# Performance work log

Measured on AMD Instinct MI355X. Metric: run time of the kernel, lower is better.

## Reference

```python
import jax, jax.numpy as jnp
import numpy as np
import math

B, Hs, Ws, C, NH, PP = 4, 32, 32, 1024, 16, 128
N = Hs * Ws
HD = C // NH
MAX_REL = 32
ROPE_THETA = 10000.0


def _gelu(t):
    return jax.nn.gelu(t, approximate=False)  # torch nn.GELU default (erf)


def _rope(x):
    # x: [B, nh, N, hd]; interleaved even/odd rotation as in _apply_rope
    hd = x.shape[-1]
    inv_freq = 1.0 / (ROPE_THETA ** (jnp.arange(0, hd, 2, dtype=jnp.float32) / hd))
    pos = jnp.arange(x.shape[-2], dtype=jnp.float32)
    ang = pos[:, None] * inv_freq[None, :]  # [N, hd/2]
    sin, cos = jnp.sin(ang), jnp.cos(ang)
    x1, x2 = x[..., 0::2], x[..., 1::2]
    return jnp.stack([x1 * cos - x2 * sin, x2 * cos + x1 * sin], axis=-1).reshape(x.shape)


def _rel_bias(table):
    # static index computation (numpy), gather from learned table -> [1, NH, N, N]
    coords = np.arange(Hs)
    cy, cx = np.meshgrid(coords, coords, indexing='ij')
    cf = np.stack([cy.reshape(-1), cx.reshape(-1)])  # [2, N]
    rel = cf[:, :, None] - cf[:, None, :]            # [2, N, N]
    idx = (rel[0] + MAX_REL - 1) * (2 * MAX_REL - 1) + (rel[1] + MAX_REL - 1)
    return table[jnp.asarray(idx.reshape(-1))].reshape(N, N, NH).transpose(2, 0, 1)[None]


def setup_inputs() -> dict:
    key = jax.random.key(0)
    ks = iter(jax.random.split(key, 40))
    def w(shape, s=0.02):
        return jax.random.normal(next(ks), shape, jnp.float32) * s
    return dict(
        x=jax.random.normal(next(ks), (B, N, C), jnp.float32),
        plucker=jax.random.normal(next(ks), (B, Hs, Ws, 6), jnp.float32),
        w_qkv=w((C, 3 * C)), w_self_proj=w((C, C)), b_self_proj=jnp.zeros((C,), jnp.float32),
        pl_w1=w((6, 2 * PP)), pl_b1=jnp.zeros((2 * PP,), jnp.float32),
        pl_w2=w((2 * PP, PP)), pl_b2=jnp.zeros((PP,), jnp.float32),
        pl_w3=w((PP, PP)), pl_b3=jnp.zeros((PP,), jnp.float32),
        w_cq=w((C, C)), w_pk=w((PP, C)), w_pv=w((PP, C)),
        w_cross_proj=w((C, C)), b_cross_proj=jnp.zeros((C,), jnp.float32),
        ray_dir_bias=w((NH,)),
        ds_w1=w((6, 4 * NH)), ds_b1=jnp.zeros((4 * NH,), jnp.float32),
        ds_w2=w((4 * NH, NH)), ds_b2=jnp.zeros((NH,), jnp.float32),
        gb_w1=w((2 * PP, C // 2)), gb_b1=jnp.zeros((C // 2,), jnp.float32),
        gb_w2=w((C // 2, NH)), gb_b2=jnp.zeros((NH,), jnp.float32),
        rel_table=w(((2 * MAX_REL - 1) ** 2, NH)),
        gfe_w1=w((C + PP, C)), gfe_b1=jnp.zeros((C,), jnp.float32),
        gfe_w2=w((C, C)), gfe_b2=jnp.zeros((C,), jnp.float32),
    )


def reference(x, plucker, w_qkv, w_self_proj, b_self_proj,
              pl_w1, pl_b1, pl_w2, pl_b2, pl_w3, pl_b3,
              w_cq, w_pk, w_pv, w_cross_proj, b_cross_proj,
              ray_dir_bias, ds_w1, ds_b1, ds_w2, ds_b2,
              gb_w1, gb_b1, gb_w2, gb_b2, rel_table,
              gfe_w1, gfe_b1, gfe_w2, gfe_b2):
    scale = HD ** (-0.5)
    pl_flat = plucker.reshape(B, N, 6)

    # ---- self attention with RoPE + relative position bias ----
    qkv = (x @ w_qkv).reshape(B, N, 3, NH, HD).transpose(2, 0, 3, 1, 4)
    q, k, v = qkv[0], qkv[1], qkv[2]          # [B, NH, N, HD]
    q, k = _rope(q), _rope(k)
    attn = jnp.einsum('bhnd,bhmd->bhnm', q, k) * scale + _rel_bias(rel_table)
    attn = jax.nn.softmax(attn, axis=-1)
    sa = jnp.einsum('bhnm,bhmd->bhnd', attn, v).transpose(0, 2, 1, 3).reshape(B, N, C)
    sa = sa @ w_self_proj + b_self_proj

    # ---- plucker mlp embedding ----
    pp = _gelu(pl_flat @ pl_w1 + pl_b1)
    pp = _gelu(pp @ pl_w2 + pl_b2)
    pp = pp @ pl_w3 + pl_b3                   # [B, N, PP]

    # ---- cross attention (features -> plucker) with geometric biases ----
    cq = (sa @ w_cq).reshape(B, N, NH, HD).transpose(0, 2, 1, 3)
    ck = (pp @ w_pk).reshape(B, N, NH, HD).transpose(0, 2, 1, 3)
    cv = (pp @ w_pv).reshape(B, N, NH, HD).transpose(0, 2, 1, 3)
    cq, ck = _rope(cq), _rope(ck)
    ca = jnp.einsum('bhnd,bhmd->bhnm', cq, ck) * scale

    # ray direction similarity bias (per-head learned weight)
    d = pl_flat[..., :3]
    dn = d / jnp.maximum(jnp.linalg.norm(d, axis=-1, keepdims=True), 1e-12)
    sim = jnp.einsum('bnd,bmd->bnm', dn, dn)  # [B, N, N]
    ca = ca + sim[:, None, :, :] * ray_dir_bias[None, :, None, None]

    # distance-aware per-query multiplicative scale
    ds = jnp.tanh(_gelu(pl_flat @ ds_w1 + ds_b1) @ ds_w2 + ds_b2)  # [B, N, NH]
    ca = ca * (1.0 + ds.transpose(0, 2, 1)[..., None])

    # geometric attention bias from spatial diffs of plucker features
    p2 = pp.reshape(B, Hs, Ws, PP)
    hdiff = jnp.pad(jnp.abs(p2[:, :, 1:] - p2[:, :, :-1]), ((0, 0), (0, 0), (0, 1), (0, 0)))
    vdiff = jnp.pad(jnp.abs(p2[:, 1:] - p2[:, :-1]), ((0, 0), (0, 1), (0, 0), (0, 0)))
    sd = jnp.concatenate([hdiff, vdiff], axis=-1).reshape(B, N, 2 * PP)
    gb = jnp.tanh(_gelu(sd @ gb_w1 + gb_b1) @ gb_w2 + gb_b2)  # [B, N, NH]
    ca = ca + gb.transpose(0, 2, 1)[:, :, None, :]            # broadcast over queries

    ca = jax.nn.softmax(ca, axis=-1)
    co = jnp.einsum('bhnm,bhmd->bhnd', ca, cv).transpose(0, 2, 1, 3).reshape(B, N, C)
    co = co @ w_cross_proj + b_cross_proj

    # ---- geometric feature enhancement + residual ----
    enh = _gelu(jnp.concatenate([co, pp], axis=-1) @ gfe_w1 + gfe_b1) @ gfe_w2 + gfe_b2
    return enh + x
```

## Files before the change

kernel.cpp:

```cpp
#include <hip/hip_runtime.h>
#include <math.h>

#define B_ 4
#define N_ 1024
#define C_ 1024
#define NH_ 16
#define HD_ 64
#define PP_ 128
#define LOG2E 1.4426950408889634f

typedef __bf16 bf16;
typedef __attribute__((ext_vector_type(8))) __bf16 bf16x8;
typedef __attribute__((ext_vector_type(4))) __bf16 bf16x4;
typedef __attribute__((ext_vector_type(4))) float f32x4;

#define MFMA_BF16(a, b, c) __builtin_amdgcn_mfma_f32_16x16x32_bf16((a), (b), (c), 0, 0, 0)

__device__ __forceinline__ float gelu_f(float x) {
    return 0.5f * x * (1.0f + erff(x * 0.70710678118654752f));
}

__device__ __forceinline__ void gload16(const void* g, void* l) {
    __builtin_amdgcn_global_load_lds(
        (const __attribute__((address_space(1))) void*)g,
        (__attribute__((address_space(3))) void*)l, 16, 0, 0);
}

__device__ __forceinline__ void stage64(const bf16* __restrict__ g, int pitchB,
                                        bf16* lds, int t) {
    int row = t >> 3, c = t & 7;
    const char* src = (const char*)g + (size_t)row * pitchB + ((c ^ (row & 7)) << 4);
    gload16(src, lds + (size_t)(t & 448) * 8);
}

__device__ __forceinline__ void stage32(const bf16* __restrict__ g, bf16* lds, int t) {
    if (t < 256) {
        int row = t >> 3, c = t & 7;
        const char* src = (const char*)g + (size_t)row * 128 + ((c ^ (row & 7)) << 4);
        gload16(src, lds + (size_t)(t & 192) * 8);
    }
}

__device__ __forceinline__ bf16x8 lds8_swz(const bf16* lds, int row, int colb) {
    return *reinterpret_cast<const bf16x8*>(
        (const char*)lds + row * 128 + (colb ^ ((row & 7) << 4)));
}

__device__ __forceinline__ bf16x8 lds8_swz256(const bf16* lds, int row, int colb) {
    return *reinterpret_cast<const bf16x8*>(
        (const char*)lds + row * 256 + (colb ^ ((row & 7) << 4)));
}

__device__ __forceinline__ bf16x8 lds8_ke(const bf16* lds, int kr, int g) {
    int r = kr >> 1;
    int ch = ((kr & 1) * 4 + g) ^ (r & 7);
    return *reinterpret_cast<const bf16x8*>((const char*)lds + r * 128 + (ch << 4));
}

struct TJobs {
    const float* src[11];
    bf16* dst[11];
    int K[11];
    int N[11];
    int base[12];
};

__global__ __launch_bounds__(256) void pre_k(
    TJobs J, const float* __restrict__ x, bf16* __restrict__ xb,
    const float* __restrict__ w_cp, bf16* __restrict__ wcpB,
    const float* __restrict__ rel_table, float* __restrict__ relT, float2* __restrict__ rt,
    const float* __restrict__ b_cp, const float* __restrict__ gfw1,
    const float* __restrict__ gfb1, float* __restrict__ bscg,
    const float* __restrict__ pl,
    const float* __restrict__ w1, const float* __restrict__ b1,
    const float* __restrict__ dw1, const float* __restrict__ db1,
    const float* __restrict__ dw2, const float* __restrict__ db2,
    bf16* __restrict__ h1b, float* __restrict__ ds, float* __restrict__ dn)
{
    __shared__ float tl[32][33];
    __shared__ float plr[6];
    __shared__ float dh[64];
    __shared__ float red[4][64];
    const int t = threadIdx.x;
    const int bid = blockIdx.x;
    const int ntc = J.base[11];
    if (bid < ntc) {
        int tile = bid;
        int j = 0;
        while (j + 1 < 11 && tile >= J.base[j + 1]) ++j;
        tile -= J.base[j];
        const int Kd = J.K[j], Nd = J.N[j];
        const int ntx = Nd >> 5;
        const int n0 = (tile % ntx) * 32, k0 = (tile / ntx) * 32;
        const int tx = t & 31, ty = t >> 5;
        const float* src = J.src[j];
        bf16* dst = J.dst[j];
        #pragma unroll
        for (int r = 0; r < 4; ++r) {
            int kk = ty + r * 8;
            tl[kk][tx] = src[(size_t)(k0 + kk) * Nd + n0 + tx];
        }
        __syncthreads();
        #pragma unroll
        for (int r = 0; r < 4; ++r) {
            int nn = ty + r * 8;
            dst[(size_t)(n0 + nn) * Kd + k0 + tx] = (bf16)tl[tx][nn];
        }
    } else if (bid < ntc + 4096) {
        int g = (bid - ntc) * 256 + t;
        float4 v = reinterpret_cast<const float4*>(x)[g];
        bf16x4 o = {(bf16)v.x, (bf16)v.y, (bf16)v.z, (bf16)v.w};
        reinterpret_cast<bf16x4*>(xb)[g] = o;
    } else if (bid < ntc + 4096 + 256) {
        int g = (bid - ntc - 4096) * 256 + t;
        float4 v = reinterpret_cast<const float4*>(w_cp)[g];
        bf16x4 o = {(bf16)v.x, (bf16)v.y, (bf16)v.z, (bf16)v.w};
        reinterpret_cast<bf16x4*>(wcpB)[g] = o;
    } else if (bid < ntc + 4096 + 256 + 377) {
        int g = (bid - ntc - 4096 - 256) * 256 + t;
        if (g < 32768) {
            const int n = g >> 5, i = g & 31;
            const float inv = powf(10000.0f, -(float)(2 * i) / 64.0f);
            const float ang = (float)n * inv;
            rt[g] = make_float2(cosf(ang), sinf(ang));
        } else {
            int i = g - 32768;
            if (i < 16 * 3969) {
                int h = i / 3969, idx = i - h * 3969;
                relT[i] = rel_table[idx * 16 + h];
            }
        }
    } else if (bid < ntc + 4096 + 256 + 377 + 16) {
        const int pb = bid - ntc - 4096 - 256 - 377;
        const int c = pb * 64 + (t & 63);
        const int js = t >> 6;
        float a = 0.f;
        #pragma unroll 8
        for (int j = js * 256; j < js * 256 + 256; ++j)
            a = fmaf(b_cp[j], gfw1[(size_t)j * 1024 + c], a);
        red[js][t & 63] = a;
        __syncthreads();
        if (t < 64) {
            int cc = pb * 64 + t;
            bscg[cc] = red[0][t] + red[1][t] + red[2][t] + red[3][t] + gfb1[cc];
        }
    } else {
        const int pb = bid - ntc - 4096 - 256 - 377 - 16;
        #pragma unroll 1
        for (int rr = 0; rr < 4; ++rr) {
            const int row = pb * 4 + rr;
            if (t < 6) plr[t] = pl[(size_t)row * 6 + t];
            __syncthreads();
            {
                float a = b1[t];
                #pragma unroll
                for (int j = 0; j < 6; ++j) a = fmaf(plr[j], w1[j * 256 + t], a);
                h1b[(size_t)row * 256 + t] = (bf16)gelu_f(a);
            }
            if (t < 64) {
                float d = db1[t];
                #pragma unroll
                for (int j = 0; j < 6; ++j) d = fmaf(plr[j], dw1[j * 64 + t], d);
                dh[t] = gelu_f(d);
            }
            if (t == 0) {
                float xx = plr[0], yy = plr[1], zz = plr[2];
                float nrm = fmaxf(sqrtf(xx * xx + yy * yy + zz * zz), 1e-12f);
                dn[(size_t)row * 4 + 0] = xx / nrm;
                dn[(size_t)row * 4 + 1] = yy / nrm;
                dn[(size_t)row * 4 + 2] = zz / nrm;
                dn[(size_t)row * 4 + 3] = 0.f;
            }
            __syncthreads();
            if (t < 16) {
                float d = db2[t];
                #pragma unroll 8
                for (int j = 0; j < 64; ++j) d = fmaf(dh[j], dw2[j * 16 + t], d);
                ds[(size_t)row * 16 + t] = tanhf(d);
            }
            __syncthreads();
        }
    }
}

struct GJob {
    const bf16* A; const bf16* A2; const bf16* Bt; const bf16* Bt2;
    const float* bias; const float* resid;
    void* out0; void* out1; void* out2;
    const float2* rtab;
    int N, K, K1A, K1B, epi, act_gelu, gx;
    float scale;
};

__device__ __forceinline__ void gemm_body(const GJob& P, int bx, int by, char* smem)
{
    const bf16* A = P.A; const bf16* A2 = P.A2;
    const bf16* Bt = P.Bt; const bf16* Bt2 = P.Bt2;
    const float* bias = P.bias; const float* resid = P.resid;
    void* out0 = P.out0; void* out1 = P.out1; void* out2 = P.out2;
    const float2* rtab = P.rtab;
    const int N = P.N, K = P.K, K1A = P.K1A, K1B = P.K1B;
    const int epi = P.epi, act_gelu = P.act_gelu;
    const float scale = P.scale;

    bf16 (*As)[128 * 64] = (bf16(*)[128 * 64])smem;
    bf16 (*Bs)[64 * 64]  = (bf16(*)[64 * 64])(smem + 32768);
    const int t = threadIdx.x;
    const int w = t >> 6, lane = t & 63;
    const int row0 = by * 128, col0 = bx * 64;
    const int wm = w >> 1, wn = w & 1;
    const int K2A = K - K1A, K2B = K - K1B;
    f32x4 acc[4][2];
    #pragma unroll
    for (int mi = 0; mi < 4; ++mi)
        #pragma unroll
        for (int ni = 0; ni < 2; ++ni)
            acc[mi][ni] = (f32x4){0.f, 0.f, 0.f, 0.f};

    #define STAGE_AB64(k0, buf)                                                \
        {                                                                      \
            const bf16* abase; int apitch;                                     \
            if ((k0) < K1A) { abase = A + (k0); apitch = K1A; }                \
            else            { abase = A2 + ((k0) - K1A); apitch = K2A; }       \
            _Pragma("unroll")                                                  \
            for (int r = 0; r < 4; ++r) {                                      \
                int c = r * 256 + t;                                           \
                int rr = c >> 3, cc = c & 7;                                   \
                const char* srca = (const char*)(abase + (size_t)(row0 + rr) * apitch) \
                                   + ((cc ^ (rr & 7)) << 4);                   \
                gload16(srca, As[buf] + (size_t)(r * 256 + (t & 192)) * 8);    \
            }                                                                  \
            const bf16* bbase; int bpitch;                                     \
            if ((k0) < K1B) { bbase = Bt + (k0); bpitch = K1B; }               \
            else            { bbase = Bt2 + ((k0) - K1B); bpitch = K2B; }      \
            _Pragma("unroll")                                                  \
            for (int r = 0; r < 2; ++r) {                                      \
                int c = r * 256 + t;                                           \
                int rr = c >> 3, cc = c & 7;                                   \
                const char* srcb = (const char*)(bbase + (size_t)(col0 + rr) * bpitch) \
                                   + ((cc ^ (rr & 7)) << 4);                   \
                gload16(srcb, Bs[buf] + (size_t)(r * 256 + (t & 192)) * 8);    \
            }                                                                  \
        }

    int cur = 0;
    const int nk = K >> 6;
    STAGE_AB64(0, 0);
    __syncthreads();
    for (int kk = 0; kk < nk; ++kk) {
        if (kk + 1 < nk) STAGE_AB64((kk + 1) * 64, cur ^ 1);
        bf16x8 af[4][2], bfv[2][2];
        #pragma unroll
        for (int mi = 0; mi < 4; ++mi)
            #pragma unroll
            for (int kh = 0; kh < 2; ++kh)
                af[mi][kh] = lds8_swz(As[cur], wm * 64 + mi * 16 + (lane & 15),
                                      kh * 64 + (lane >> 4) * 16);
        #pragma unroll
        for (int ni = 0; ni < 2; ++ni)
            #pragma unroll
            for (int kh = 0; kh < 2; ++kh)
                bfv[ni][kh] = lds8_swz(Bs[cur], wn * 32 + ni * 16 + (lane & 15),
                                       kh * 64 + (lane >> 4) * 16);
        #pragma unroll
        for (int kh = 0; kh < 2; ++kh)
            #pragma unroll
            for (int mi = 0; mi < 4; ++mi)
                #pragma unroll
                for (int ni = 0; ni < 2; ++ni)
                    acc[mi][ni] = MFMA_BF16(af[mi][kh], bfv[ni][kh], acc[mi][ni]);
        __syncthreads();
        cur ^= 1;
    }
    #undef STAGE_AB64

    #pragma unroll
    for (int mi = 0; mi < 4; ++mi) {
        #pragma unroll
        for (int ni = 0; ni < 2; ++ni) {
            const int col = col0 + wn * 32 + ni * 16 + (lane & 15);
            if (epi <= 1 || epi == 5) {
                const float bv = bias ? bias[col] : 0.f;
                #pragma unroll
                for (int j = 0; j < 4; ++j) {
                    const int row = row0 + wm * 64 + mi * 16 + (lane >> 4) * 4 + j;
                    float v = acc[mi][ni][j] + bv;
                    if (act_gelu) v = gelu_f(v);
                    if (epi == 0) {
                        if (resid) v += resid[(size_t)row * N + col];
                        ((float*)out0)[(size_t)row * N + col] = v;
                    } else if (epi == 1) {
                        ((bf16*)out0)[(size_t)row * N + col] = (bf16)v;
                    } else {
                        ((float*)out0)[(size_t)row * N + col] = v;
                        ((bf16*)out1)[(size_t)row * N + col] = (bf16)v;
                    }
                }
            } else if (epi == 2) {
                const int reg = col >> 10;
                const int h = (col >> 6) & 15, d = col & 63;
                if (reg <= 1) {
                    bf16* dst = reg == 0 ? (bf16*)out0 : (bf16*)out1;
                    const float sc = reg == 0 ? scale : 1.0f;
                    #pragma unroll
                    for (int j = 0; j < 4; ++j) {
                        const int row = row0 + wm * 64 + mi * 16 + (lane >> 4) * 4 + j;
                        const int b = row >> 10, n = row & 1023;
                        float v = acc[mi][ni][j];
                        float pv = __shfl_xor(v, 1);
                        float2 cs = rtab[(n << 5) + (d >> 1)];
                        float o = (d & 1) == 0 ? v * cs.x - pv * cs.y
                                               : v * cs.x + pv * cs.y;
                        dst[((size_t)((b * 16 + h) * 1024 + n)) * 64 + d] = (bf16)(o * sc);
                    }
                } else {
                    bf16x4 o4;
                    #pragma unroll
                    for (int j = 0; j < 4; ++j) o4[j] = (bf16)acc[mi][ni][j];
                    const int row = row0 + wm * 64 + mi * 16 + (lane >> 4) * 4;
                    const int b = row >> 10, n = row & 1023;
                    *reinterpret_cast<bf16x4*>(
                        (bf16*)out2 + ((size_t)((b * 16 + h) * 64 + d)) * 1024 + n) = o4;
                }
            } else if (epi == 3 || epi == 6) {
                const int h = (col >> 6) & 15, d = col & 63;
                const float bv = bias ? bias[col] : 0.f;
                #pragma unroll
                for (int j = 0; j < 4; ++j) {
                    const int row = row0 + wm * 64 + mi * 16 + (lane >> 4) * 4 + j;
                    const int b = row >> 10, n = row & 1023;
                    float v = acc[mi][ni][j] + bv;
                    float pv = __shfl_xor(v, 1);
                    float2 cs = rtab[(n << 5) + (d >> 1)];
                    float o = (d & 1) == 0 ? v * cs.x - pv * cs.y
                                           : v * cs.x + pv * cs.y;
                    float sc = scale;
                    if (epi == 6) sc *= 1.0f + resid[(size_t)row * 16 + h];
                    ((bf16*)out0)[((size_t)((b * 16 + h) * 1024 + n)) * 64 + d] = (bf16)(o * sc);
                }
            } else if (epi == 7) {
                const int reg = col >> 10;
                const int h = (col >> 6) & 15, d = col & 63;
                if (reg == 0) {
                    #pragma unroll
                    for (int j = 0; j < 4; ++j) {
                        const int row = row0 + wm * 64 + mi * 16 + (lane >> 4) * 4 + j;
                        const int b = row >> 10, n = row & 1023;
                        float v = acc[mi][ni][j];
                        float pv = __shfl_xor(v, 1);
                        float2 cs = rtab[(n << 5) + (d >> 1)];
                        float o = (d & 1) == 0 ? v * cs.x - pv * cs.y
                                               : v * cs.x + pv * cs.y;
                        ((bf16*)out0)[((size_t)((b * 16 + h) * 1024 + n)) * 64 + d] = (bf16)o;
                    }
                } else {
                    bf16x4 o4;
                    #pragma unroll
                    for (int j = 0; j < 4; ++j) o4[j] = (bf16)acc[mi][ni][j];
                    const int row = row0 + wm * 64 + mi * 16 + (lane >> 4) * 4;
                    const int b = row >> 10, n = row & 1023;
                    *reinterpret_cast<bf16x4*>(
                        (bf16*)out2 + ((size_t)((b * 16 + h) * 64 + d)) * 1024 + n) = o4;
                }
            } else {
                const int h = (col >> 6) & 15, d = col & 63;
                bf16x4 o4;
                #pragma unroll
                for (int j = 0; j < 4; ++j) o4[j] = (bf16)acc[mi][ni][j];
                const int row = row0 + wm * 64 + mi * 16 + (lane >> 4) * 4;
                const int b = row >> 10, n = row & 1023;
                *reinterpret_cast<bf16x4*>(
                    (bf16*)out0 + ((size_t)((b * 16 + h) * 64 + d)) * 1024 + n) = o4;
            }
        }
    }
}

__device__ __forceinline__ void pl23m_body(
    int bid, const bf16* __restrict__ h1, const bf16* __restrict__ w2T,
    const float* __restrict__ b2, const bf16* __restrict__ w3T, const float* __restrict__ b3,
    float* __restrict__ pp, bf16* __restrict__ ppb, char* smem)
{
    bf16* Am = (bf16*)smem;
    bf16* Wm = (bf16*)(smem + 16384);
    const int t = threadIdx.x, w = t >> 6, lane = t & 63;
    const int row0 = bid * 64;
    f32x4 acc[8];
    #pragma unroll
    for (int nt = 0; nt < 8; ++nt) acc[nt] = (f32x4){0.f, 0.f, 0.f, 0.f};

    for (int kc = 0; kc < 2; ++kc) {
        #pragma unroll
        for (int r = 0; r < 4; ++r) {
            int i = r * 256 + t;
            int row = i >> 4, c = i & 15;
            const char* src = (const char*)(h1 + (size_t)(row0 + row) * 256 + kc * 128)
                              + ((c ^ (row & 7)) << 4);
            gload16(src, Am + (size_t)(r * 256 + (t & 192)) * 8);
        }
        #pragma unroll
        for (int r = 0; r < 8; ++r) {
            int i = r * 256 + t;
            int row = i >> 4, c = i & 15;
            const char* src = (const char*)(w2T + (size_t)row * 256 + kc * 128)
                              + ((c ^ (row & 7)) << 4);
            gload16(src, Wm + (size_t)(r * 256 + (t & 192)) * 8);
        }
        __syncthreads();
        #pragma unroll
        for (int step = 0; step < 4; ++step) {
            bf16x8 af = lds8_swz256(Am, w * 16 + (lane & 15), step * 64 + (lane >> 4) * 16);
            #pragma unroll
            for (int nt = 0; nt < 8; ++nt) {
                bf16x8 bfv = lds8_swz256(Wm, nt * 16 + (lane & 15), step * 64 + (lane >> 4) * 16);
                acc[nt] = MFMA_BF16(af, bfv, acc[nt]);
            }
        }
        __syncthreads();
    }
    #pragma unroll
    for (int r = 0; r < 8; ++r) {
        int i = r * 256 + t;
        int row = i >> 4, c = i & 15;
        const char* src = (const char*)(w3T + (size_t)row * 128) + ((c ^ (row & 7)) << 4);
        gload16(src, Wm + (size_t)(r * 256 + (t & 192)) * 8);
    }
    #pragma unroll
    for (int nt = 0; nt < 8; ++nt) {
        const int col = nt * 16 + (lane & 15);
        const float bv = b2[col];
        #pragma unroll
        for (int j = 0; j < 4; ++j) {
            const int row = w * 16 + (lane >> 4) * 4 + j;
            const int byte = row * 256 + (((col * 2) & ~15) ^ ((row & 7) << 4)) + ((col * 2) & 15);
            *reinterpret_cast<bf16*>((char*)Am + byte) = (bf16)gelu_f(acc[nt][j] + bv);
        }
    }
    __syncthreads();
    f32x4 acc2[8];
    #pragma unroll
    for (int nt = 0; nt < 8; ++nt) acc2[nt] = (f32x4){0.f, 0.f, 0.f, 0.f};
    #pragma unroll
    for (int step = 0; step < 4; ++step) {
        bf16x8 af = lds8_swz256(Am, w * 16 + (lane & 15), step * 64 + (lane >> 4) * 16);
        #pragma unroll
        for (int nt = 0; nt < 8; ++nt) {
            bf16x8 bfv = lds8_swz256(Wm, nt * 16 + (lane & 15), step * 64 + (lane >> 4) * 16);
            acc2[nt] = MFMA_BF16(af, bfv, acc2[nt]);
        }
    }
    #pragma unroll
    for (int nt = 0; nt < 8; ++nt) {
        const int col = nt * 16 + (lane & 15);
        const float bv = b3[col];
        #pragma unroll
        for (int j = 0; j < 4; ++j) {
            const int row = row0 + w * 16 + (lane >> 4) * 4 + j;
            const float v = acc2[nt][j] + bv;
            pp[(size_t)row * 128 + col] = v;
            ppb[(size_t)row * 128 + col] = (bf16)v;
        }
    }
}

__device__ __forceinline__ void gb2x_body(
    int bid, const bf16* __restrict__ h, const float* __restrict__ w2,
    const float* __restrict__ b2, const float* __restrict__ dn,
    const float* __restrict__ ds, const float* __restrict__ rdb,
    bf16* __restrict__ qe, bf16* __restrict__ ke, char* smem)
{
    float* w2s = (float*)smem;
    const int t = threadIdx.x;
    for (int i = t; i < 8192; i += 256) w2s[i] = w2[i];
    __syncthreads();
    const int row = bid * 16 + (t >> 4);
    const int hh = t & 15;
    const bf16* hr = h + (size_t)row * 512;
    float acc = b2[hh];
    #pragma unroll 8
    for (int j = 0; j < 512; ++j)
        acc = fmaf((float)hr[j], w2s[j * 16 + hh], acc);
    const float gbv = tanhf(acc);
    const int b = row >> 10, n = row & 1023;
    const float c1 = rdb[hh] * LOG2E * (1.0f + ds[(size_t)row * 16 + hh]);
    const float dx = dn[(size_t)row * 4], dy = dn[(size_t)row * 4 + 1], dz = dn[(size_t)row * 4 + 2];
    bf16x8 z = {};
    bf16x8 q0 = z, k0 = z;
    q0[0] = (bf16)(dx * c1); q0[1] = (bf16)(dy * c1); q0[2] = (bf16)(dz * c1); q0[3] = (bf16)1.0f;
    k0[0] = (bf16)dx; k0[1] = (bf16)dy; k0[2] = (bf16)dz; k0[3] = (bf16)(gbv * LOG2E);
    const size_t g = (size_t)(b * 16 + hh) * 1024 + n;
    bf16x8* qp = reinterpret_cast<bf16x8*>(qe + g * 32);
    bf16x8* kp = reinterpret_cast<bf16x8*>(ke + g * 32);
    qp[0] = q0; qp[1] = z; qp[2] = z; qp[3] = z;
    kp[0] = k0; kp[1] = z; kp[2] = z; kp[3] = z;
}

__global__ __launch_bounds__(256) void gemm_k(GJob P)
{
    __shared__ char smem[49152];
    gemm_body(P, blockIdx.x % P.gx, blockIdx.x / P.gx, smem);
}

__global__ __launch_bounds__(256) void gemm2_k(GJob P0, GJob P1, int split)
{
    __shared__ char smem[49152];
    int id = blockIdx.x;
    if (id < split) gemm_body(P0, id % P0.gx, id / P0.gx, smem);
    else {
        id -= split;
        gemm_body(P1, id % P1.gx, id / P1.gx, smem);
    }
}

__global__ __launch_bounds__(256) void qkvpl_k(GJob P, GJob Pc,
    const bf16* __restrict__ h1, const bf16* __restrict__ w2T, const float* __restrict__ b2,
    const bf16* __restrict__ w3T, const float* __restrict__ b3,
    float* __restrict__ pp, bf16* __restrict__ ppb)
{
    __shared__ char smem[49152];
    if (blockIdx.x < 128) gemm_body(Pc, blockIdx.x % Pc.gx, blockIdx.x / Pc.gx, smem);
    else if (blockIdx.x < 192) pl23m_body(blockIdx.x - 128, h1, w2T, b2, w3T, b3, pp, ppb, smem);
    else {
        int id = blockIdx.x - 192;
        gemm_body(P, id % P.gx, id / P.gx, smem);
    }
}

__global__ __launch_bounds__(256) void gemm2gb_k(GJob P0, GJob P1,
    const bf16* __restrict__ h, const float* __restrict__ w2, const float* __restrict__ b2,
    const float* __restrict__ dn, const float* __restrict__ ds, const float* __restrict__ rdb,
    bf16* __restrict__ qe, bf16* __restrict__ ke)
{
    __shared__ char smem[49152];
    int id = blockIdx.x;
    if (id < 256) gb2x_body(id, h, w2, b2, dn, ds, rdb, qe, ke, smem);
    else if (id < 768) {
        id -= 256;
        gemm_body(P0, id % P0.gx, id / P0.gx, smem);
    } else {
        id -= 768;
        gemm_body(P1, id % P1.gx, id / P1.gx, smem);
    }
}

__device__ __forceinline__ void attn_bid(int bid, int& bh, int& r0t) {
    const int xcd = bid & 7, s = bid >> 3;
    bh = (s >> 3) * 8 + xcd;
    r0t = s & 7;
}

__global__ __launch_bounds__(512) void attnsd_k(
    const bf16* __restrict__ qb, const bf16* __restrict__ kb, const bf16* __restrict__ vtb,
    const float* __restrict__ relT, bf16* __restrict__ sab,
    const float* __restrict__ pp, bf16* __restrict__ sd)
{
    __shared__ bf16 Ks[2][64 * 64];
    __shared__ bf16 Vs[2][80 * 64];
    __shared__ bf16 Ps[128 * 64];
    __shared__ float relb[2][320];
    const int t = threadIdx.x, w = t >> 6, lane = t & 63;
    if (blockIdx.x >= 512) {
        int g = (blockIdx.x - 512) * 512 + t;
        if (g < B_ * N_ * PP_) {
            const int c = g & 127;
            const int rown = g >> 7;
            const int n = rown & (N_ - 1);
            const int xx = n & 31, yy = (n >> 5) & 31;
            const float cur = pp[g];
            const float hd = (xx < 31) ? fabsf(pp[g + PP_] - cur) : 0.f;
            const float vd = (yy < 31) ? fabsf(pp[g + 32 * PP_] - cur) : 0.f;
            sd[(size_t)rown * 256 + c] = (bf16)hd;
            sd[(size_t)rown * 256 + 128 + c] = (bf16)vd;
        }
        return;
    }
    int bh, r0t;
    attn_bid(blockIdx.x, bh, r0t);
    const int b = bh >> 4, h = bh & 15, r0 = r0t * 128;
    const float* relTh = relT + h * 3969;
    const int y0 = r0 >> 5;

    {
        const bf16* g = qb + ((size_t)bh * 1024 + r0) * 64;
        #pragma unroll
        for (int r = 0; r < 2; ++r) {
            int i = r * 512 + t;
            int row = i >> 3, c = i & 7;
            const char* src = (const char*)g + (size_t)row * 128 + ((c ^ (row & 7)) << 4);
            gload16(src, Ps + (size_t)(r * 512 + (t & 448)) * 8);
        }
    }
    __syncthreads();
    bf16x8 aq[2];
    {
        const int qr = w * 16 + (lane & 15);
        aq[0] = lds8_swz(Ps, qr, (lane >> 4) * 16);
        aq[1] = lds8_swz(Ps, qr, 64 + (lane >> 4) * 16);
    }
    for (int i = t; i < 2048; i += 512) {
        int buf = i >> 10, idx = i & 1023;
        int row = 64 + (idx >> 6), col = idx & 63;
        Vs[buf][row * 64 + col] = (row == 64) ? (bf16)1.0f : (bf16)0.0f;
    }
    __syncthreads();
    stage64(kb + (size_t)bh * 65536, 128, Ks[0], t);
    stage64(vtb + (size_t)bh * 65536, 2048, Vs[0], t);
    if (t < 320) relb[0][t] = LOG2E * relTh[(y0 + 30 + (t >> 6)) * 63 + min(t & 63, 62)];

    float m_run[4];
    f32x4 of[4], ofe;
    #pragma unroll
    for (int j = 0; j < 4; ++j) m_run[j] = -3e38f;
    #pragma unroll
    for (int dt = 0; dt < 4; ++dt) of[dt] = (f32x4){0.f, 0.f, 0.f, 0.f};
    ofe = (f32x4){0.f, 0.f, 0.f, 0.f};

    const int qrow_lo = (lane >> 4) * 4;
    int dybase[4];
    #pragma unroll
    for (int j = 0; j < 4; ++j) {
        int qg = r0 + w * 16 + qrow_lo + j;
        dybase[j] = (((qg >> 5) - y0) + 1) * 64 + (qg & 31) + 31;
    }
    __syncthreads();

    int cur = 0;
    for (int mt = 0; mt < 16; ++mt) {
        if (mt < 15) {
            stage64(kb + (size_t)bh * 65536 + (size_t)(mt + 1) * 64 * 64, 128, Ks[cur ^ 1], t);
            stage64(vtb + (size_t)bh * 65536 + (size_t)(mt + 1) * 64, 2048, Vs[cur ^ 1], t);
            if (t < 320)
                relb[cur ^ 1][t] = LOG2E * relTh[(y0 - 2 * (mt + 1) + 30 + (t >> 6)) * 63 + min(t & 63, 62)];
        }
        f32x4 sf[4];
        __builtin_amdgcn_s_setprio(1);
        #pragma unroll
        for (int ct = 0; ct < 4; ++ct) {
            const int kr = ct * 16 + (lane & 15);
            f32x4 a = (f32x4){0.f, 0.f, 0.f, 0.f};
            a = MFMA_BF16(aq[0], lds8_swz(Ks[cur], kr, (lane >> 4) * 16), a);
            a = MFMA_BF16(aq[1], lds8_swz(Ks[cur], kr, 64 + (lane >> 4) * 16), a);
            sf[ct] = a;
        }
        __builtin_amdgcn_s_setprio(0);
        float p[4][4], lmax[4];
        #pragma unroll
        for (int j = 0; j < 4; ++j) lmax[j] = -3e38f;
        #pragma unroll
        for (int ct = 0; ct < 4; ++ct) {
            const int xm = (ct & 1) * 16 + (lane & 15);
            const int ro = (ct >> 1) * 64 + xm;
            #pragma unroll
            for (int j = 0; j < 4; ++j) {
                float s = sf[ct][j] + relb[cur][dybase[j] - ro];
                p[ct][j] = s;
                lmax[j] = fmaxf(lmax[j], s);
            }
        }
        bool need = false;
        #pragma unroll
        for (int j = 0; j < 4; ++j) need |= (lmax[j] > m_run[j] + 8.0f);
        if (__any(need)) {
            float mx[4], alpha[4];
            #pragma unroll
            for (int j = 0; j < 4; ++j) mx[j] = lmax[j];
            #pragma unroll
            for (int d = 1; d < 16; d <<= 1)
                #pragma unroll
                for (int j = 0; j < 4; ++j) mx[j] = fmaxf(mx[j], __shfl_xor(mx[j], d));
            #pragma unroll
            for (int j = 0; j < 4; ++j) {
                float mn = fmaxf(m_run[j], mx[j]);
                alpha[j] = exp2f(m_run[j] - mn);
                m_run[j] = mn;
            }
            #pragma unroll
            for (int dt = 0; dt < 4; ++dt)
                #pragma unroll
                for (int j = 0; j < 4; ++j) of[dt][j] *= alpha[j];
            #pragma unroll
            for (int j = 0; j < 4; ++j) ofe[j] *= alpha[j];
        }
        #pragma unroll
        for (int ct = 0; ct < 4; ++ct)
            #pragma unroll
            for (int j = 0; j < 4; ++j)
                p[ct][j] = exp2f(p[ct][j] - m_run[j]);
        #pragma unroll
        for (int ct = 0; ct < 4; ++ct)
            #pragma unroll
            for (int j = 0; j < 4; ++j) {
                const int prow = w * 16 + qrow_lo + j;
                const int ch = (ct * 2 + ((lane & 15) >> 3)) ^ (prow & 7);
                *reinterpret_cast<bf16*>((char*)Ps + prow * 128 + (ch << 4) + (lane & 7) * 2)
                    = (bf16)p[ct][j];
            }
        asm volatile("s_waitcnt lgkmcnt(0)" ::: "memory");
        __builtin_amdgcn_sched_barrier(0);
        bf16x8 ap0 = lds8_swz(Ps, w * 16 + (lane & 15), (lane >> 4) * 16);
        bf16x8 ap1 = lds8_swz(Ps, w * 16 + (lane & 15), 64 + (lane >> 4) * 16);
        __builtin_amdgcn_s_setprio(1);
        #pragma unroll
        for (int dt = 0; dt < 4; ++dt) {
            const int vr = dt * 16 + (lane & 15);
            of[dt] = MFMA_BF16(ap0, lds8_swz(Vs[cur], vr, (lane >> 4) * 16), of[dt]);
            of[dt] = MFMA_BF16(ap1, lds8_swz(Vs[cur], vr, 64 + (lane >> 4) * 16), of[dt]);
        }
        {
            const int vr = 64 + (lane & 15);
            ofe = MFMA_BF16(ap0, lds8_swz(Vs[cur], vr, (lane >> 4) * 16), ofe);
            ofe = MFMA_BF16(ap1, lds8_swz(Vs[cur], vr, 64 + (lane >> 4) * 16), ofe);
        }
        __builtin_amdgcn_s_setprio(0);
        __syncthreads();
        cur ^= 1;
    }
    float inv[4];
    #pragma unroll
    for (int j = 0; j < 4; ++j) inv[j] = 1.f / __shfl(ofe[j], lane & 48);
    #pragma unroll
    for (int dt = 0; dt < 4; ++dt)
        #pragma unroll
        for (int j = 0; j < 4; ++j)
            sab[((size_t)(b * N_ + r0 + w * 16 + qrow_lo + j)) * C_ + h * 64 + dt * 16 + (lane & 15)] =
                (bf16)(of[dt][j] * inv[j]);
}

__global__ __launch_bounds__(512) void attn_cross_m(
    const bf16* __restrict__ cq, const bf16* __restrict__ qe,
    const bf16* __restrict__ ck, const bf16* __restrict__ ke,
    const bf16* __restrict__ cvt, bf16* __restrict__ cob)
{
    __shared__ bf16 Ks[2][64 * 64];
    __shared__ bf16 Ke[2][32 * 64];
    __shared__ bf16 Vs[2][80 * 64];
    __shared__ bf16 Ps[128 * 64];
    const int t = threadIdx.x, w = t >> 6, lane = t & 63;
    int bh, r0t;
    attn_bid(blockIdx.x, bh, r0t);
    const int b = bh >> 4, h = bh & 15, r0 = r0t * 128;

    {
        const bf16* g = cq + ((size_t)bh * 1024 + r0) * 64;
        #pragma unroll
        for (int r = 0; r < 2; ++r) {
            int i = r * 512 + t;
            int row = i >> 3, c = i & 7;
            const char* src = (const char*)g + (size_t)row * 128 + ((c ^ (row & 7)) << 4);
            gload16(src, Ps + (size_t)(r * 512 + (t & 448)) * 8);
        }
    }
    stage64(qe + ((size_t)bh * 1024 + r0) * 32, 128, Ks[0], t);
    __syncthreads();
    bf16x8 aq[2], aqe;
    {
        const int qr = w * 16 + (lane & 15);
        aq[0] = lds8_swz(Ps, qr, (lane >> 4) * 16);
        aq[1] = lds8_swz(Ps, qr, 64 + (lane >> 4) * 16);
        aqe = lds8_ke(Ks[0], qr, lane >> 4);
    }
    for (int i = t; i < 2048; i += 512) {
        int buf = i >> 10, idx = i & 1023;
        int row = 64 + (idx >> 6), col = idx & 63;
        Vs[buf][row * 64 + col] = (row == 64) ? (bf16)1.0f : (bf16)0.0f;
    }
    __syncthreads();
    stage64(ck + (size_t)bh * 65536, 128, Ks[0], t);
    stage32(ke + (size_t)bh * 32768, Ke[0], t);
    stage64(cvt + (size_t)bh * 65536, 2048, Vs[0], t);

    float m_run[4];
    f32x4 of[4], ofe;
    #pragma unroll
    for (int j = 0; j < 4; ++j) m_run[j] = -3e38f;
    #pragma unroll
    for (int dt = 0; dt < 4; ++dt) of[dt] = (f32x4){0.f, 0.f, 0.f, 0.f};
    ofe = (f32x4){0.f, 0.f, 0.f, 0.f};
    const int qrow_lo = (lane >> 4) * 4;
    __syncthreads();

    int cur = 0;
    for (int mt = 0; mt < 16; ++mt) {
        if (mt < 15) {
            stage64(ck + (size_t)bh * 65536 + (size_t)(mt + 1) * 64 * 64, 128, Ks[cur ^ 1], t);
            stage32(ke + (size_t)bh * 32768 + (size_t)(mt + 1) * 64 * 32, Ke[cur ^ 1], t);
            stage64(cvt + (size_t)bh * 65536 + (size_t)(mt + 1) * 64, 2048, Vs[cur ^ 1], t);
        }
        f32x4 sf[4];
        __builtin_amdgcn_s_setprio(1);
        #pragma unroll
        for (int ct = 0; ct < 4; ++ct) {
            const int kr = ct * 16 + (lane & 15);
            f32x4 a = (f32x4){0.f, 0.f, 0.f, 0.f};
            a = MFMA_BF16(aq[0], lds8_swz(Ks[cur], kr, (lane >> 4) * 16), a);
            a = MFMA_BF16(aq[1], lds8_swz(Ks[cur], kr, 64 + (lane >> 4) * 16), a);
            a = MFMA_BF16(aqe, lds8_ke(Ke[cur], kr, lane >> 4), a);
            sf[ct] = a;
        }
        __builtin_amdgcn_s_setprio(0);
        float lmax[4];
        #pragma unroll
        for (int j = 0; j < 4; ++j)
            lmax[j] = fmaxf(fmaxf(sf[0][j], sf[1][j]), fmaxf(sf[2][j], sf[3][j]));
        bool need = false;
        #pragma unroll
        for (int j = 0; j < 4; ++j) need |= (lmax[j] > m_run[j] + 8.0f);
        if (__any(need)) {
            float mx[4], alpha[4];
            #pragma unroll
            for (int j = 0; j < 4; ++j) mx[j] = lmax[j];
            #pragma unroll
            for (int d = 1; d < 16; d <<= 1)
                #pragma unroll
                for (int j = 0; j < 4; ++j) mx[j] = fmaxf(mx[j], __shfl_xor(mx[j], d));
            #pragma unroll
            for (int j = 0; j < 4; ++j) {
                float mn = fmaxf(m_run[j], mx[j]);
                alpha[j] = exp2f(m_run[j] - mn);
                m_run[j] = mn;
            }
            #pragma unroll
            for (int dt = 0; dt < 4; ++dt)
                #pragma unroll
                for (int j = 0; j < 4; ++j) of[dt][j] *= alpha[j];
            #pragma unroll
            for (int j = 0; j < 4; ++j) ofe[j] *= alpha[j];
        }
        #pragma unroll
        for (int ct = 0; ct < 4; ++ct)
            #pragma unroll
            for (int j = 0; j < 4; ++j)
                sf[ct][j] = exp2f(sf[ct][j] - m_run[j]);
        #pragma unroll
        for (int ct = 0; ct < 4; ++ct)
            #pragma unroll
            for (int j = 0; j < 4; ++j) {
                const int prow = w * 16 + qrow_lo + j;
                const int ch = (ct * 2 + ((lane & 15) >> 3)) ^ (prow & 7);
                *reinterpret_cast<bf16*>((char*)Ps + prow * 128 + (ch << 4) + (lane & 7) * 2)
                    = (bf16)sf[ct][j];
            }
        asm volatile("s_waitcnt lgkmcnt(0)" ::: "memory");
        __builtin_amdgcn_sched_barrier(0);
        bf16x8 ap0 = lds8_swz(Ps, w * 16 + (lane & 15), (lane >> 4) * 16);
        bf16x8 ap1 = lds8_swz(Ps, w * 16 + (lane & 15), 64 + (lane >> 4) * 16);
        __builtin_amdgcn_s_setprio(1);
        #pragma unroll
        for (int dt = 0; dt < 4; ++dt) {
            const int vr = dt * 16 + (lane & 15);
            of[dt] = MFMA_BF16(ap0, lds8_swz(Vs[cur], vr, (lane >> 4) * 16), of[dt]);
            of[dt] = MFMA_BF16(ap1, lds8_swz(Vs[cur], vr, 64 + (lane >> 4) * 16), of[dt]);
        }
        {
            const int vr = 64 + (lane & 15);
            ofe = MFMA_BF16(ap0, lds8_swz(Vs[cur], vr, (lane >> 4) * 16), ofe);
            ofe = MFMA_BF16(ap1, lds8_swz(Vs[cur], vr, 64 + (lane >> 4) * 16), ofe);
        }
        __builtin_amdgcn_s_setprio(0);
        __syncthreads();
        cur ^= 1;
    }
    float inv[4];
    #pragma unroll
    for (int j = 0; j < 4; ++j) inv[j] = 1.f / __shfl(ofe[j], lane & 48);
    #pragma unroll
    for (int dt = 0; dt < 4; ++dt)
        #pragma unroll
        for (int j = 0; j < 4; ++j)
            cob[((size_t)(b * N_ + r0 + w * 16 + qrow_lo + j)) * C_ + h * 64 + dt * 16 + (lane & 15)] =
                (bf16)(of[dt][j] * inv[j]);
}

extern "C" void kernel_launch(void* const* d_in, const int* in_sizes, int n_in,
                              void* d_out, int out_size, void* d_ws, size_t ws_size,
                              hipStream_t stream)
{
    const float* x     = (const float*)d_in[0];
    const float* pl    = (const float*)d_in[1];
    const float* w_qkv = (const float*)d_in[2];
    const float* w_sp  = (const float*)d_in[3];
    const float* b_sp  = (const float*)d_in[4];
    const float* pl_w1 = (const float*)d_in[5];
    const float* pl_b1 = (const float*)d_in[6];
    const float* pl_w2 = (const float*)d_in[7];
    const float* pl_b2 = (const float*)d_in[8];
    const float* pl_w3 = (const float*)d_in[9];
    const float* pl_b3 = (const float*)d_in[10];
    const float* w_cq  = (const float*)d_in[11];
    const float* w_pk  = (const float*)d_in[12];
    const float* w_pv  = (const float*)d_in[13];
    const float* w_cp  = (const float*)d_in[14];
    const float* b_cp  = (const float*)d_in[15];
    const float* rdb   = (const float*)d_in[16];
    const float* ds_w1 = (const float*)d_in[17];
    const float* ds_b1 = (const float*)d_in[18];
    const float* ds_w2 = (const float*)d_in[19];
    const float* ds_b2 = (const float*)d_in[20];
    const float* gb_w1 = (const float*)d_in[21];
    const float* gb_b1 = (const float*)d_in[22];
    const float* gb_w2 = (const float*)d_in[23];
    const float* gb_b2 = (const float*)d_in[24];
    const float* rel_t = (const float*)d_in[25];
    const float* gfw1  = (const float*)d_in[26];
    const float* gfb1  = (const float*)d_in[27];
    const float* gfw2  = (const float*)d_in[28];
    const float* gfb2  = (const float*)d_in[29];

    char* W = (char*)d_ws;
    float* out = (float*)d_out;
    const size_t MB = 1ull << 20;
    const size_t KB = 1024;

    bf16* qb     = (bf16*)(W + 0);
    bf16* kb     = (bf16*)(W + 8 * MB);
    bf16* vtb    = (bf16*)(W + 16 * MB);
    bf16* cqb    = qb;
    bf16* ckb    = kb;
    bf16* cvtb   = vtb;
    bf16* xb     = (bf16*)(W + 24 * MB);
    bf16* wqkvT  = (bf16*)(W + 32 * MB);
    bf16* wspT   = (bf16*)(W + 38 * MB);
    bf16* wcqT   = (bf16*)(W + 40 * MB);
    bf16* wpkT   = (bf16*)(W + 42 * MB);
    bf16* wpvT   = (bf16*)(W + 42 * MB + 256 * KB);
    bf16* wcpB   = (bf16*)(W + 43 * MB);
    bf16* gf1tT  = (bf16*)(W + 45 * MB);
    bf16* gf1bT  = (bf16*)(W + 47 * MB);
    bf16* gfw2T  = (bf16*)(W + 48 * MB);
    bf16* gbw1T  = (bf16*)(W + 50 * MB);
    bf16* plw2T  = (bf16*)(W + 50 * MB + 256 * KB);
    bf16* plw3T  = (bf16*)(W + 50 * MB + 320 * KB);
    bf16* sab    = (bf16*)(W + 51 * MB);
    bf16* cob    = sab;
    bf16* sapb   = (bf16*)(W + 59 * MB);
    float* pp    = (float*)(W + 67 * MB);
    bf16* ppb    = (bf16*)(W + 69 * MB);
    bf16* sdb16  = (bf16*)(W + 70 * MB);
    bf16* h1b    = (bf16*)(W + 72 * MB);
    bf16* gbh    = (bf16*)(W + 75 * MB);
    float* dsb   = (float*)(W + 79 * MB);
    float* dnb   = (float*)(W + 79 * MB + 256 * KB);
    float2* rtab = (float2*)(W + 80 * MB);
    float* relTb = (float*)(W + 80 * MB + 256 * KB);
    bf16* hidb   = (bf16*)(W + 81 * MB);
    bf16* qeb    = (bf16*)(W + 89 * MB);
    bf16* keb    = (bf16*)(W + 93 * MB);
    bf16* wcgT   = (bf16*)(W + 97 * MB);
    float* bscgb = (float*)(W + 99 * MB);

    const dim3 blk(256);

    TJobs J;
    J.src[0] = w_qkv;              J.dst[0] = wqkvT; J.K[0] = 1024; J.N[0] = 3072;
    J.src[1] = w_sp;               J.dst[1] = wspT;  J.K[1] = 1024; J.N[1] = 1024;
    J.src[2] = w_cq;               J.dst[2] = wcqT;  J.K[2] = 1024; J.N[2] = 1024;
    J.src[3] = w_pk;               J.dst[3] = wpkT;  J.K[3] = 128;  J.N[3] = 1024;
    J.src[4] = w_pv;               J.dst[4] = wpvT;  J.K[4] = 128;  J.N[4] = 1024;
    J.src[5] = gfw1;               J.dst[5] = gf1tT; J.K[5] = 1024; J.N[5] = 1024;
    J.src[6] = gfw1 + 1024 * 1024; J.dst[6] = gf1bT; J.K[6] = 128;  J.N[6] = 1024;
    J.src[7] = gfw2;               J.dst[7] = gfw2T; J.K[7] = 1024; J.N[7] = 1024;
    J.src[8] = gb_w1;              J.dst[8] = gbw1T; J.K[8] = 256;  J.N[8] = 512;
    J.src[9] = pl_w2;              J.dst[9] = plw2T; J.K[9] = 256;  J.N[9] = 128;
    J.src[10]= pl_w3;              J.dst[10]= plw3T; J.K[10]= 128;  J.N[10]= 128;
    {
        int acc = 0;
        for (int j = 0; j < 11; ++j) {
            J.base[j] = acc;
            acc += (J.N[j] >> 5) * (J.K[j] >> 5);
        }
        J.base[11] = acc;
    }
    const int pre_blocks = J.base[11] + 4096 + 256 + 377 + 16 + 1024;

    auto mkjob = [](const bf16* A, const bf16* A2, const bf16* Bt, const bf16* Bt2,
                    const float* bias, const float* resid,
                    void* o0, void* o1, void* o2, const float2* rt,
                    int N, int K, int K1A, int K1B, int epi, int ag, int gx, float sc) {
        GJob g;
        g.A = A; g.A2 = A2; g.Bt = Bt; g.Bt2 = Bt2; g.bias = bias; g.resid = resid;
        g.out0 = o0; g.out1 = o1; g.out2 = o2; g.rtab = rt;
        g.N = N; g.K = K; g.K1A = K1A; g.K1B = K1B; g.epi = epi; g.act_gelu = ag;
        g.gx = gx; g.scale = sc;
        return g;
    };

    pre_k<<<pre_blocks, blk, 0, stream>>>(J, x, xb, w_cp, wcpB, rel_t, relTb, rtab,
        b_cp, gfw1, gfb1, bscgb,
        pl, pl_w1, pl_b1, ds_w1, ds_b1, ds_w2, ds_b2, h1b, dsb, dnb);
    GJob jqkv = mkjob(xb, nullptr, wqkvT, nullptr, nullptr, nullptr,
                      qb, kb, vtb, rtab, 3072, 1024, 1024, 1024, 2, 0, 48, 0.125f * LOG2E);
    GJob jwcg = mkjob(gf1tT, nullptr, wcpB, nullptr, nullptr, nullptr,
                      wcgT, nullptr, nullptr, nullptr, 1024, 1024, 1024, 1024, 1, 0, 16, 1.f);
    qkvpl_k<<<128 + 64 + 1536, blk, 0, stream>>>(jqkv, jwcg,
        h1b, plw2T, pl_b2, plw3T, pl_b3, pp, ppb);
    attnsd_k<<<512 + 1024, dim3(512), 0, stream>>>(qb, kb, vtb, relTb, sab, pp, sdb16);
    GJob jgb1 = mkjob(sdb16, nullptr, gbw1T, nullptr, gb_b1, nullptr,
                      gbh, nullptr, nullptr, nullptr, 512, 256, 256, 256, 1, 1, 8, 1.f);
    GJob jsp  = mkjob(sab, nullptr, wspT, nullptr, b_sp, nullptr,
                      sapb, nullptr, nullptr, nullptr, 1024, 1024, 1024, 1024, 1, 0, 16, 1.f);
    gemm2_k<<<256 + 512, blk, 0, stream>>>(jgb1, jsp, 256);
    GJob jcq  = mkjob(sapb, nullptr, wcqT, nullptr, nullptr, dsb,
                      cqb, nullptr, nullptr, rtab, 1024, 1024, 1024, 1024, 6, 0, 16, 0.125f * LOG2E);
    GJob jkcv = mkjob(ppb, nullptr, wpkT, nullptr, nullptr, nullptr,
                      ckb, nullptr, cvtb, rtab, 2048, 128, 128, 128, 7, 0, 32, 1.f);
    gemm2gb_k<<<256 + 512 + 1024, blk, 0, stream>>>(jcq, jkcv,
        gbh, gb_w2, gb_b2, dnb, dsb, rdb, qeb, keb);
    attn_cross_m<<<512, dim3(512), 0, stream>>>(cqb, qeb, ckb, keb, cvtb, cob);
    GJob jg1 = mkjob(cob, ppb, wcgT, gf1bT, bscgb, nullptr,
                     hidb, nullptr, nullptr, nullptr, 1024, 1152, 1024, 1024, 1, 1, 16, 1.f);
    gemm_k<<<512, blk, 0, stream>>>(jg1);
    GJob jg2 = mkjob(hidb, nullptr, gfw2T, nullptr, gfb2, x,
                     out, nullptr, nullptr, nullptr, 1024, 1024, 1024, 1024, 0, 0, 16, 1.f);
    gemm_k<<<512, blk, 0, stream>>>(jg2);
}
```

Measured before the change: 290.2 us.

## Fold self-projection into cross-query weights to drop an activation GEMM

Precomputes the product of the self-projection and cross-query weights, plus the bias term b_sp·W_cq, inside the preprocessing and first GEMM kernels. The cross-query GEMM then consumes the self-attention output directly. This removes the full 4096x1024x1024 self-projection GEMM on activations and its intermediate buffer. In exchange it adds a 1024^3 weight GEMM that runs alongside the QKV GEMM, and it adds a second bf16 rounding of the combined weight.

```diff
diff --git a/kernel.cpp b/kernel.cpp
--- a/kernel.cpp
+++ b/kernel.cpp
@@ -68,9 +68,11 @@
 __global__ __launch_bounds__(256) void pre_k(
     TJobs J, const float* __restrict__ x, bf16* __restrict__ xb,
     const float* __restrict__ w_cp, bf16* __restrict__ wcpB,
+    const float* __restrict__ w_sp, bf16* __restrict__ wspB,
     const float* __restrict__ rel_table, float* __restrict__ relT, float2* __restrict__ rt,
     const float* __restrict__ b_cp, const float* __restrict__ gfw1,
     const float* __restrict__ gfb1, float* __restrict__ bscg,
+    const float* __restrict__ b_sp, const float* __restrict__ w_cq, float* __restrict__ bsc,
     const float* __restrict__ pl,
     const float* __restrict__ w1, const float* __restrict__ b1,
     const float* __restrict__ dw1, const float* __restrict__ db1,
@@ -83,11 +85,11 @@
     __shared__ float red[4][64];
     const int t = threadIdx.x;
     const int bid = blockIdx.x;
-    const int ntc = J.base[11];
+    const int ntc = J.base[10];
     if (bid < ntc) {
         int tile = bid;
         int j = 0;
-        while (j + 1 < 11 && tile >= J.base[j + 1]) ++j;
+        while (j + 1 < 10 && tile >= J.base[j + 1]) ++j;
         tile -= J.base[j];
         const int Kd = J.K[j], Nd = J.N[j];
         const int ntx = Nd >> 5;
@@ -116,8 +118,13 @@
         float4 v = reinterpret_cast<const float4*>(w_cp)[g];
         bf16x4 o = {(bf16)v.x, (bf16)v.y, (bf16)v.z, (bf16)v.w};
         reinterpret_cast<bf16x4*>(wcpB)[g] = o;
-    } else if (bid < ntc + 4096 + 256 + 377) {
+    } else if (bid < ntc + 4096 + 512) {
         int g = (bid - ntc - 4096 - 256) * 256 + t;
+        float4 v = reinterpret_cast<const float4*>(w_sp)[g];
+        bf16x4 o = {(bf16)v.x, (bf16)v.y, (bf16)v.z, (bf16)v.w};
+        reinterpret_cast<bf16x4*>(wspB)[g] = o;
+    } else if (bid < ntc + 4096 + 512 + 377) {
+        int g = (bid - ntc - 4096 - 512) * 256 + t;
         if (g < 32768) {
             const int n = g >> 5, i = g & 31;
             const float inv = powf(10000.0f, -(float)(2 * i) / 64.0f);
@@ -130,8 +137,8 @@
                 relT[i] = rel_table[idx * 16 + h];
             }
         }
-    } else if (bid < ntc + 4096 + 256 + 377 + 16) {
-        const int pb = bid - ntc - 4096 - 256 - 377;
+    } else if (bid < ntc + 4096 + 512 + 377 + 16) {
+        const int pb = bid - ntc - 4096 - 512 - 377;
         const int c = pb * 64 + (t & 63);
         const int js = t >> 6;
         float a = 0.f;
@@ -144,8 +151,22 @@
             int cc = pb * 64 + t;
             bscg[cc] = red[0][t] + red[1][t] + red[2][t] + red[3][t] + gfb1[cc];
         }
+    } else if (bid < ntc + 4096 + 512 + 377 + 32) {
+        const int pb = bid - ntc - 4096 - 512 - 377 - 16;
+        const int c = pb * 64 + (t & 63);
+        const int js = t >> 6;
+        float a = 0.f;
+        #pragma unroll 8
+        for (int j = js * 256; j < js * 256 + 256; ++j)
+            a = fmaf(b_sp[j], w_cq[(size_t)j * 1024 + c], a);
+        red[js][t & 63] = a;
+        __syncthreads();
+        if (t < 64) {
+            int cc = pb * 64 + t;
+            bsc[cc] = red[0][t] + red[1][t] + red[2][t] + red[3][t];
+        }
     } else {
-        const int pb = bid - ntc - 4096 - 256 - 377 - 16;
+        const int pb = bid - ntc - 4096 - 512 - 377 - 32;
         #pragma unroll 1
         for (int rr = 0; rr < 4; ++rr) {
             const int row = pb * 4 + rr;
@@ -501,27 +522,19 @@
     gemm_body(P, blockIdx.x % P.gx, blockIdx.x / P.gx, smem);
 }
 
-__global__ __launch_bounds__(256) void gemm2_k(GJob P0, GJob P1, int split)
-{
-    __shared__ char smem[49152];
-    int id = blockIdx.x;
-    if (id < split) gemm_body(P0, id % P0.gx, id / P0.gx, smem);
-    else {
-        id -= split;
-        gemm_body(P1, id % P1.gx, id / P1.gx, smem);
-    }
-}
-
-__global__ __launch_bounds__(256) void qkvpl_k(GJob P, GJob Pc,
+__global__ __launch_bounds__(256) void qkvpl_k(GJob P, GJob Pc, GJob Ps2,
     const bf16* __restrict__ h1, const bf16* __restrict__ w2T, const float* __restrict__ b2,
     const bf16* __restrict__ w3T, const float* __restrict__ b3,
     float* __restrict__ pp, bf16* __restrict__ ppb)
 {
     __shared__ char smem[49152];
-    if (blockIdx.x < 128) gemm_body(Pc, blockIdx.x % Pc.gx, blockIdx.x / Pc.gx, smem);
-    else if (blockIdx.x < 192) pl23m_body(blockIdx.x - 128, h1, w2T, b2, w3T, b3, pp, ppb, smem);
+    if (blockIdx.x < 128) gemm_body(Ps2, blockIdx.x % Ps2.gx, blockIdx.x / Ps2.gx, smem);
+    else if (blockIdx.x < 256) {
+        int id = blockIdx.x - 128;
+        gemm_body(Pc, id % Pc.gx, id / Pc.gx, smem);
+    } else if (blockIdx.x < 320) pl23m_body(blockIdx.x - 256, h1, w2T, b2, w3T, b3, pp, ppb, smem);
     else {
-        int id = blockIdx.x - 192;
+        int id = blockIdx.x - 320;
         gemm_body(P, id % P.gx, id / P.gx, smem);
     }
 }
@@ -919,7 +932,7 @@
     bf16* cvtb   = vtb;
     bf16* xb     = (bf16*)(W + 24 * MB);
     bf16* wqkvT  = (bf16*)(W + 32 * MB);
-    bf16* wspT   = (bf16*)(W + 38 * MB);
+    bf16* wspB   = (bf16*)(W + 38 * MB);
     bf16* wcqT   = (bf16*)(W + 40 * MB);
     bf16* wpkT   = (bf16*)(W + 42 * MB);
     bf16* wpvT   = (bf16*)(W + 42 * MB + 256 * KB);
@@ -932,7 +945,6 @@
     bf16* plw3T  = (bf16*)(W + 50 * MB + 320 * KB);
     bf16* sab    = (bf16*)(W + 51 * MB);
     bf16* cob    = sab;
-    bf16* sapb   = (bf16*)(W + 59 * MB);
     float* pp    = (float*)(W + 67 * MB);
     bf16* ppb    = (bf16*)(W + 69 * MB);
     bf16* sdb16  = (bf16*)(W + 70 * MB);
@@ -947,30 +959,31 @@
     bf16* keb    = (bf16*)(W + 93 * MB);
     bf16* wcgT   = (bf16*)(W + 97 * MB);
     float* bscgb = (float*)(W + 99 * MB);
+    float* bscb  = (float*)(W + 99 * MB + 8 * KB);
+    bf16* wscT   = (bf16*)(W + 100 * MB);
 
     const dim3 blk(256);
 
     TJobs J;
     J.src[0] = w_qkv;              J.dst[0] = wqkvT; J.K[0] = 1024; J.N[0] = 3072;
-    J.src[1] = w_sp;               J.dst[1] = wspT;  J.K[1] = 1024; J.N[1] = 1024;
-    J.src[2] = w_cq;               J.dst[2] = wcqT;  J.K[2] = 1024; J.N[2] = 1024;
-    J.src[3] = w_pk;               J.dst[3] = wpkT;  J.K[3] = 128;  J.N[3] = 1024;
-    J.src[4] = w_pv;               J.dst[4] = wpvT;  J.K[4] = 128;  J.N[4] = 1024;
-    J.src[5] = gfw1;               J.dst[5] = gf1tT; J.K[5] = 1024; J.N[5] = 1024;
-    J.src[6] = gfw1 + 1024 * 1024; J.dst[6] = gf1bT; J.K[6] = 128;  J.N[6] = 1024;
-    J.src[7] = gfw2;               J.dst[7] = gfw2T; J.K[7] = 1024; J.N[7] = 1024;
-    J.src[8] = gb_w1;              J.dst[8] = gbw1T; J.K[8] = 256;  J.N[8] = 512;
-    J.src[9] = pl_w2;              J.dst[9] = plw2T; J.K[9] = 256;  J.N[9] = 128;
-    J.src[10]= pl_w3;              J.dst[10]= plw3T; J.K[10]= 128;  J.N[10]= 128;
+    J.src[1] = w_cq;               J.dst[1] = wcqT;  J.K[1] = 1024; J.N[1] = 1024;
+    J.src[2] = w_pk;               J.dst[2] = wpkT;  J.K[2] = 128;  J.N[2] = 1024;
+    J.src[3] = w_pv;               J.dst[3] = wpvT;  J.K[3] = 128;  J.N[3] = 1024;
+    J.src[4] = gfw1;               J.dst[4] = gf1tT; J.K[4] = 1024; J.N[4] = 1024;
+    J.src[5] = gfw1 + 1024 * 1024; J.dst[5] = gf1bT; J.K[5] = 128;  J.N[5] = 1024;
+    J.src[6] = gfw2;               J.dst[6] = gfw2T; J.K[6] = 1024; J.N[6] = 1024;
+    J.src[7] = gb_w1;              J.dst[7] = gbw1T; J.K[7] = 256;  J.N[7] = 512;
+    J.src[8] = pl_w2;              J.dst[8] = plw2T; J.K[8] = 256;  J.N[8] = 128;
+    J.src[9] = pl_w3;              J.dst[9] = plw3T; J.K[9] = 128;  J.N[9] = 128;
     {
         int acc = 0;
-        for (int j = 0; j < 11; ++j) {
+        for (int j = 0; j < 10; ++j) {
             J.base[j] = acc;
             acc += (J.N[j] >> 5) * (J.K[j] >> 5);
         }
-        J.base[11] = acc;
-    }
-    const int pre_blocks = J.base[11] + 4096 + 256 + 377 + 16 + 1024;
+        J.base[10] = acc;
+    }
+    const int pre_blocks = J.base[10] + 4096 + 512 + 377 + 32 + 1024;
 
     auto mkjob = [](const bf16* A, const bf16* A2, const bf16* Bt, const bf16* Bt2,
                     const float* bias, const float* resid,
@@ -984,22 +997,22 @@
         return g;
     };
 
-    pre_k<<<pre_blocks, blk, 0, stream>>>(J, x, xb, w_cp, wcpB, rel_t, relTb, rtab,
-        b_cp, gfw1, gfb1, bscgb,
+    pre_k<<<pre_blocks, blk, 0, stream>>>(J, x, xb, w_cp, wcpB, w_sp, wspB,
+        rel_t, relTb, rtab, b_cp, gfw1, gfb1, bscgb, b_sp, w_cq, bscb,
         pl, pl_w1, pl_b1, ds_w1, ds_b1, ds_w2, ds_b2, h1b, dsb, dnb);
     GJob jqkv = mkjob(xb, nullptr, wqkvT, nullptr, nullptr, nullptr,
                       qb, kb, vtb, rtab, 3072, 1024, 1024, 1024, 2, 0, 48, 0.125f * LOG2E);
     GJob jwcg = mkjob(gf1tT, nullptr, wcpB, nullptr, nullptr, nullptr,
                       wcgT, nullptr, nullptr, nullptr, 1024, 1024, 1024, 1024, 1, 0, 16, 1.f);
-    qkvpl_k<<<128 + 64 + 1536, blk, 0, stream>>>(jqkv, jwcg,
+    GJob jwsc = mkjob(wcqT, nullptr, wspB, nullptr, nullptr, nullptr,
+                      wscT, nullptr, nullptr, nullptr, 1024, 1024, 1024, 1024, 1, 0, 16, 1.f);
+    qkvpl_k<<<128 + 128 + 64 + 1536, blk, 0, stream>>>(jqkv, jwcg, jwsc,
         h1b, plw2T, pl_b2, plw3T, pl_b3, pp, ppb);
     attnsd_k<<<512 + 1024, dim3(512), 0, stream>>>(qb, kb, vtb, relTb, sab, pp, sdb16);
     GJob jgb1 = mkjob(sdb16, nullptr, gbw1T, nullptr, gb_b1, nullptr,
                       gbh, nullptr, nullptr, nullptr, 512, 256, 256, 256, 1, 1, 8, 1.f);
-    GJob jsp  = mkjob(sab, nullptr, wspT, nullptr, b_sp, nullptr,
-                      sapb, nullptr, nullptr, nullptr, 1024, 1024, 1024, 1024, 1, 0, 16, 1.f);
-    gemm2_k<<<256 + 512, blk, 0, stream>>>(jgb1, jsp, 256);
-    GJob jcq  = mkjob(sapb, nullptr, wcqT, nullptr, nullptr, dsb,
+    gemm_k<<<256, blk, 0, stream>>>(jgb1);
+    GJob jcq  = mkjob(sab, nullptr, wscT, nullptr, bscb, dsb,
                       cqb, nullptr, nullptr, rtab, 1024, 1024, 1024, 1024, 6, 0, 16, 0.125f * LOG2E);
     GJob jkcv = mkjob(ppb, nullptr, wpkT, nullptr, nullptr, nullptr,
                       ckb, nullptr, cvtb, rtab, 2048, 128, 128, 128, 7, 0, 32, 1.f);
```

Result: faster. 281.9 us, median of 2 (-2.9%).
